# Kernel optimization log

Measured on AMD Instinct MI355X. Metric: run time of the kernel, lower is better.

## Reference

```python
import jax, jax.numpy as jnp
import numpy as np


def setup_inputs() -> dict:
    key = jax.random.key(0)
    k1, k2, k3 = jax.random.split(key, 3)
    B, T, C = 16, 8192, 128  # batch, tokens, max_columns
    column_logits = jax.random.normal(k1, (B, T, C), dtype=jnp.float32)
    column_assignments = jax.random.randint(k2, (B, T), 0, C)
    valid_mask = jax.random.randint(k3, (B, T), 0, 2).astype(bool)
    return {
        "column_logits": column_logits,
        "column_assignments": column_assignments,
        "valid_mask": valid_mask,
    }


def reference(column_logits, column_assignments, valid_mask):
    # column_logits: (B, T, C); column_assignments: (B, T) int; valid_mask: (B, T) bool
    B, T, C = column_logits.shape
    probs = jax.nn.softmax(column_logits, axis=-1).reshape(-1, C)  # (N, C)
    seg = column_assignments.reshape(-1)                           # (N,)
    w = valid_mask.reshape(-1).astype(probs.dtype)                 # (N,)

    # Single-pass segmented stats over column ids (num_segments = max_columns).
    n = jax.ops.segment_sum(w, seg, num_segments=C)                       # (C,)
    s = jax.ops.segment_sum(probs * w[:, None], seg, num_segments=C)      # (C, C)
    n_safe = jnp.maximum(n, 1.0)
    mean = s / n_safe[:, None]                                            # per-column mean prob

    # Sum of squared deviations (matches torch's ((p - mean)**2).mean()).
    diff = probs - mean[seg]
    ssd = jax.ops.segment_sum((diff * diff) * w[:, None], seg, num_segments=C)  # (C, C)
    col_var = ssd.sum(axis=-1) / (n_safe * C)                                    # (C,)

    has_multi = n > 1.0  # columns with at least 2 valid tokens
    count = has_multi.sum().astype(col_var.dtype)
    total = jnp.where(has_multi, col_var, 0.0).sum()
    return jnp.where(count > 0, total / jnp.maximum(count, 1.0), 0.0)
```

## Files before the change

kernel.cpp:

```cpp
#include <hip/hip_runtime.h>
#include <hip/hip_bf16.h>


#define NROWS 131072
#define CC    128
#define NB    256
#define RPB   512

typedef float f32x16 __attribute__((ext_vector_type(16)));
typedef short bf16x8 __attribute__((ext_vector_type(8)));

union U4V { uint4 u; bf16x8 v; };
union H2U { __hip_bfloat162 h; unsigned int u; };

__global__ __launch_bounds__(1024) void fused_kernel(
    const float* __restrict__ logits, const int* __restrict__ seg,
    const int* __restrict__ mask, float* __restrict__ slab_s,
    float* __restrict__ slab_n, float* __restrict__ slab_q,
    float* __restrict__ acc) {
  __shared__ ushort Plds[RPB * CC];
  __shared__ int sm[RPB];
  __shared__ unsigned int sg4[128];
  __shared__ float n_lds[CC], q_lds[CC];
  const int t = threadIdx.x, b = blockIdx.x;
  if (b == 0 && t < 4) ((unsigned int*)acc)[t] = 0u;
  if (t < CC) { n_lds[t] = 0.f; q_lds[t] = 0.f; }
  if (t < RPB) {
    const int r = b * RPB + t;
    sm[t] = seg[r] | (mask[r] << 16);
  }
  __syncthreads();
  if (t < 128) {
    unsigned int w = 0;
#pragma unroll
    for (int k = 0; k < 4; ++k) {
      const int smv = sm[t * 4 + k];
      const unsigned int sv = (smv >> 16) ? (unsigned int)(smv & 0xFFFF) : 255u;
      w |= sv << (8 * k);
    }
    sg4[t] = w;
  }

  const int wave = t >> 6, lane = t & 63;
  const int q = lane >> 5, j5 = lane & 31;
#pragma unroll
  for (int g = 0; g < 2; ++g) {
    const int ts = 2 * wave + g;
    const int rb = ts * 16 + q * 8;
    float x[8][4];
#pragma unroll
    for (int i = 0; i < 8; ++i) {
      const float* rp = logits + (size_t)(b * RPB + rb + i) * CC + j5;
#pragma unroll
      for (int nt = 0; nt < 4; ++nt) x[i][nt] = rp[nt * 32];
    }
    float inv[8], qr[8];
#pragma unroll
    for (int i = 0; i < 8; ++i) {
      float z = 0.f, z2 = 0.f;
#pragma unroll
      for (int nt = 0; nt < 4; ++nt) {
        const float e = __expf(x[i][nt]);
        x[i][nt] = e; z += e; z2 += e * e;
      }
#pragma unroll
      for (int off = 1; off < 32; off <<= 1) {
        z  += __shfl_xor(z, off, 64);
        z2 += __shfl_xor(z2, off, 64);
      }
      inv[i] = 1.0f / z;
      qr[i] = z2 * inv[i] * inv[i];
    }
#pragma unroll
    for (int nt = 0; nt < 4; ++nt) {
      unsigned int d[4];
#pragma unroll
      for (int k = 0; k < 4; ++k) {
        H2U h;
        h.h = __float22bfloat162_rn(make_float2(
            x[2 * k][nt] * inv[2 * k], x[2 * k + 1][nt] * inv[2 * k + 1]));
        d[k] = h.u;
      }
      *(uint4*)(Plds + ((size_t)(ts * 4 + nt) * 64 + lane) * 8) =
          make_uint4(d[0], d[1], d[2], d[3]);
    }
    if (j5 == 0) {
#pragma unroll
      for (int i = 0; i < 8; ++i) {
        const int smv = sm[rb + i];
        if (smv >> 16) {
          atomicAdd(&n_lds[smv & 0xFFFF], 1.0f);
          atomicAdd(&q_lds[smv & 0xFFFF], qr[i]);
        }
      }
    }
  }
  __syncthreads();

  if (t >= 256 && t < 384) slab_n[(t - 256) * NB + b] = n_lds[t - 256];
  else if (t >= 384 && t < 512) slab_q[(t - 384) * NB + b] = q_lds[t - 384];

  if (wave < 4) {
    const int mm = wave * 32 + (lane & 31);
    f32x16 acc0 = {}, acc1 = {}, acc2 = {}, acc3 = {};
    const ushort* pl = Plds + (size_t)lane * 8;
    for (int ks = 0; ks < 32; ++ks) {
      const unsigned int w0 = sg4[ks * 4 + q * 2];
      const unsigned int w1 = sg4[ks * 4 + q * 2 + 1];
      U4V a;
      {
        const unsigned int s0 = w0 & 255u, s1 = (w0 >> 8) & 255u;
        const unsigned int s2 = (w0 >> 16) & 255u, s3 = w0 >> 24;
        const unsigned int s4 = w1 & 255u, s5 = (w1 >> 8) & 255u;
        const unsigned int s6 = (w1 >> 16) & 255u, s7 = w1 >> 24;
        const unsigned int um = (unsigned int)mm;
        a.u = make_uint4(
            (s0 == um ? 0x3F80u : 0u) | (s1 == um ? 0x3F800000u : 0u),
            (s2 == um ? 0x3F80u : 0u) | (s3 == um ? 0x3F800000u : 0u),
            (s4 == um ? 0x3F80u : 0u) | (s5 == um ? 0x3F800000u : 0u),
            (s6 == um ? 0x3F80u : 0u) | (s7 == um ? 0x3F800000u : 0u));
      }
      U4V b0, b1, b2, b3;
      b0.u = *(const uint4*)(pl + (size_t)(ks * 4 + 0) * 512);
      b1.u = *(const uint4*)(pl + (size_t)(ks * 4 + 1) * 512);
      b2.u = *(const uint4*)(pl + (size_t)(ks * 4 + 2) * 512);
      b3.u = *(const uint4*)(pl + (size_t)(ks * 4 + 3) * 512);
      acc0 = __builtin_amdgcn_mfma_f32_32x32x16_bf16(a.v, b0.v, acc0, 0, 0, 0);
      acc1 = __builtin_amdgcn_mfma_f32_32x32x16_bf16(a.v, b1.v, acc1, 0, 0, 0);
      acc2 = __builtin_amdgcn_mfma_f32_32x32x16_bf16(a.v, b2.v, acc2, 0, 0, 0);
      acc3 = __builtin_amdgcn_mfma_f32_32x32x16_bf16(a.v, b3.v, acc3, 0, 0, 0);
    }
    float* outp = slab_s + (size_t)b * (CC * CC);
    const int jcol = lane & 31;
    const int rbase = (lane >> 5) * 4;
#pragma unroll
    for (int reg = 0; reg < 16; ++reg) {
      const int c = wave * 32 + (reg & 3) + 8 * (reg >> 2) + rbase;
      outp[c * CC + 0 * 32 + jcol] = acc0[reg];
      outp[c * CC + 1 * 32 + jcol] = acc1[reg];
      outp[c * CC + 2 * 32 + jcol] = acc2[reg];
      outp[c * CC + 3 * 32 + jcol] = acc3[reg];
    }
  }
}

__global__ __launch_bounds__(1024) void k3_colvar(
    const float* __restrict__ slab_s, const float* __restrict__ slab_n,
    const float* __restrict__ slab_q, float* __restrict__ acc,
    float* __restrict__ out) {
  const int c = blockIdx.x, t = threadIdx.x;
  const int v = t & 31, g0 = t >> 5;
  __shared__ float4 part[32][32];
  {
    const float4* base = (const float4*)slab_s +
                         (size_t)g0 * (CC * CC / 4) + c * (CC / 4) + v;
    float4 a = make_float4(0.f, 0.f, 0.f, 0.f);
#pragma unroll
    for (int i = 0; i < 8; ++i) {
      const float4 x = base[(size_t)(32 * i) * (CC * CC / 4)];
      a.x += x.x; a.y += x.y; a.z += x.z; a.w += x.w;
    }
    part[g0][v] = a;
  }
  float np = 0.f, qp = 0.f;
  if (t >= 64 && t < 128) {
    const int k = t - 64;
#pragma unroll
    for (int i = 0; i < 4; ++i) np += slab_n[c * NB + k + 64 * i];
  } else if (t >= 128 && t < 192) {
    const int k = t - 128;
#pragma unroll
    for (int i = 0; i < 4; ++i) qp += slab_q[c * NB + k + 64 * i];
  }
  __syncthreads();
  float tp = 0.f;
  if (t < 32) {
    float4 s = make_float4(0.f, 0.f, 0.f, 0.f);
#pragma unroll
    for (int g = 0; g < 32; ++g) {
      const float4 x = part[g][v];
      s.x += x.x; s.y += x.y; s.z += x.z; s.w += x.w;
    }
    tp = s.x * s.x + s.y * s.y + s.z * s.z + s.w * s.w;
  }
#pragma unroll
  for (int off = 1; off < 64; off <<= 1) {
    tp += __shfl_xor(tp, off, 64);
    np += __shfl_xor(np, off, 64);
    qp += __shfl_xor(qp, off, 64);
  }
  __shared__ float fin[3];
  if (t == 0) fin[0] = tp;
  else if (t == 64) fin[1] = np;
  else if (t == 128) fin[2] = qp;
  __syncthreads();
  if (t == 0) {
    const float tt = fin[0], nn = fin[1], qq = fin[2];
    float cv = 0.f, fl = 0.f;
    if (nn > 1.0f) {
      cv = (qq - tt / nn) / (nn * (float)CC);
      fl = 1.f;
    }
    atomicAdd(&acc[0], cv);
    atomicAdd(&acc[1], fl);
    __threadfence();
    const unsigned int old = atomicAdd((unsigned int*)&acc[2], 1u);
    if (old == (unsigned int)(CC - 1)) {
      const float total = atomicAdd(&acc[0], 0.f);
      const float count = atomicAdd(&acc[1], 0.f);
      out[0] = (count > 0.f) ? total / fmaxf(count, 1.f) : 0.f;
    }
  }
}

extern "C" void kernel_launch(void* const* d_in, const int* in_sizes, int n_in,
                              void* d_out, int out_size, void* d_ws,
                              size_t ws_size, hipStream_t stream) {
  const float* logits = (const float*)d_in[0];
  const int* seg = (const int*)d_in[1];
  const int* mask = (const int*)d_in[2];
  float* out = (float*)d_out;

  float* slab_s = (float*)d_ws;
  float* slab_n = slab_s + (size_t)NB * CC * CC;
  float* slab_q = slab_n + CC * NB;
  float* acc = slab_q + CC * NB;
  fused_kernel<<<NB, 1024, 0, stream>>>(logits, seg, mask, slab_s, slab_n,
                                        slab_q, acc);
  k3_colvar<<<CC, 1024, 0, stream>>>(slab_s, slab_n, slab_q, acc, out);
}
```

Measured before the change: 109.7 us.

## Pipeline softmax producers and MFMA consumers through a triple-buffered LDS ring

```diff
diff --git a/kernel.cpp b/kernel.cpp
--- a/kernel.cpp
+++ b/kernel.cpp
@@ -6,29 +6,101 @@
 #define CC    128
 #define NB    256
 #define RPB   512
+#define BUF_USHORTS (8 * 4 * 64 * 8)
 
 typedef float f32x16 __attribute__((ext_vector_type(16)));
 typedef short bf16x8 __attribute__((ext_vector_type(8)));
 
 union U4V { uint4 u; bf16x8 v; };
 union H2U { __hip_bfloat162 h; unsigned int u; };
+
+__device__ __forceinline__ float red32(float x) {
+  x += __int_as_float(__builtin_amdgcn_update_dpp(
+      0, __float_as_int(x), 0x121, 0xF, 0xF, true));
+  x += __int_as_float(__builtin_amdgcn_update_dpp(
+      0, __float_as_int(x), 0x122, 0xF, 0xF, true));
+  x += __int_as_float(__builtin_amdgcn_update_dpp(
+      0, __float_as_int(x), 0x124, 0xF, 0xF, true));
+  x += __int_as_float(__builtin_amdgcn_update_dpp(
+      0, __float_as_int(x), 0x128, 0xF, 0xF, true));
+  x += __int_as_float(
+      __builtin_amdgcn_ds_swizzle(__float_as_int(x), 0x401F));
+  return x;
+}
+
+__device__ __forceinline__ void load_x(const float* __restrict__ logits,
+                                       int b, int rb, int j5,
+                                       float (&x)[8][4]) {
+#pragma unroll
+  for (int i = 0; i < 8; ++i) {
+    const float* rp = logits + (size_t)(b * RPB + rb + i) * CC + j5;
+#pragma unroll
+    for (int nt = 0; nt < 4; ++nt) x[i][nt] = rp[nt * 32];
+  }
+}
+
+__device__ __forceinline__ void finish_ts(float (&x)[8][4], const int* sm,
+                                          float* n_lds, float* q_lds,
+                                          ushort* buf, int tsl, int rb,
+                                          int lane, int j5) {
+  float inv[8], qr[8];
+#pragma unroll
+  for (int i = 0; i < 8; ++i) {
+    float z = 0.f, z2 = 0.f;
+#pragma unroll
+    for (int nt = 0; nt < 4; ++nt) {
+      const float e = __expf(x[i][nt]);
+      x[i][nt] = e; z += e; z2 += e * e;
+    }
+    z = red32(z);
+    z2 = red32(z2);
+    inv[i] = 1.0f / z;
+    qr[i] = z2 * inv[i] * inv[i];
+  }
+#pragma unroll
+  for (int nt = 0; nt < 4; ++nt) {
+    unsigned int d[4];
+#pragma unroll
+    for (int k = 0; k < 4; ++k) {
+      H2U h;
+      h.h = __float22bfloat162_rn(make_float2(
+          x[2 * k][nt] * inv[2 * k], x[2 * k + 1][nt] * inv[2 * k + 1]));
+      d[k] = h.u;
+    }
+    *(uint4*)(buf + ((size_t)(tsl * 4 + nt) * 64 + lane) * 8) =
+        make_uint4(d[0], d[1], d[2], d[3]);
+  }
+  if (j5 == 0) {
+#pragma unroll
+    for (int i = 0; i < 8; ++i) {
+      const int smv = sm[rb + i];
+      if (smv >> 16) {
+        atomicAdd(&n_lds[smv & 0xFFFF], 1.0f);
+        atomicAdd(&q_lds[smv & 0xFFFF], qr[i]);
+      }
+    }
+  }
+}
 
 __global__ __launch_bounds__(1024) void fused_kernel(
     const float* __restrict__ logits, const int* __restrict__ seg,
     const int* __restrict__ mask, float* __restrict__ slab_s,
     float* __restrict__ slab_n, float* __restrict__ slab_q,
     float* __restrict__ acc) {
-  __shared__ ushort Plds[RPB * CC];
+  __shared__ ushort Pbuf[3][BUF_USHORTS];
   __shared__ int sm[RPB];
   __shared__ unsigned int sg4[128];
   __shared__ float n_lds[CC], q_lds[CC];
   const int t = threadIdx.x, b = blockIdx.x;
+  const int wave = t >> 6, lane = t & 63;
+  const int q = lane >> 5, j5 = lane & 31;
+
+  float x[8][4];
+  load_x(logits, b, wave * 16 + q * 8, j5, x);
+
   if (b == 0 && t < 4) ((unsigned int*)acc)[t] = 0u;
+  if (t < RPB) sm[t] = seg[b * RPB + t] | (mask[b * RPB + t] << 16);
   if (t < CC) { n_lds[t] = 0.f; q_lds[t] = 0.f; }
-  if (t < RPB) {
-    const int r = b * RPB + t;
-    sm[t] = seg[r] | (mask[r] << 16);
-  }
   __syncthreads();
   if (t < 128) {
     unsigned int w = 0;
@@ -40,106 +112,69 @@
     }
     sg4[t] = w;
   }
-
-  const int wave = t >> 6, lane = t & 63;
-  const int q = lane >> 5, j5 = lane & 31;
-#pragma unroll
-  for (int g = 0; g < 2; ++g) {
-    const int ts = 2 * wave + g;
-    const int rb = ts * 16 + q * 8;
-    float x[8][4];
-#pragma unroll
-    for (int i = 0; i < 8; ++i) {
-      const float* rp = logits + (size_t)(b * RPB + rb + i) * CC + j5;
-#pragma unroll
-      for (int nt = 0; nt < 4; ++nt) x[i][nt] = rp[nt * 32];
-    }
-    float inv[8], qr[8];
-#pragma unroll
-    for (int i = 0; i < 8; ++i) {
-      float z = 0.f, z2 = 0.f;
-#pragma unroll
-      for (int nt = 0; nt < 4; ++nt) {
-        const float e = __expf(x[i][nt]);
-        x[i][nt] = e; z += e; z2 += e * e;
+  finish_ts(x, sm, n_lds, q_lds, Pbuf[wave >> 3], wave & 7,
+            wave * 16 + q * 8, lane, j5);
+  __syncthreads();
+
+  const int ci = wave - 8;
+  const int m = ci & 3, nh = ci >> 2;
+  const int mm = m * 32 + (lane & 31);
+  f32x16 acc0 = {}, acc1 = {};
+
+#pragma unroll
+  for (int c = 0; c < 4; ++c) {
+    if (wave < 8) {
+      if (c < 2) {
+        const int ts = (c + 2) * 8 + wave;
+        float y[8][4];
+        load_x(logits, b, ts * 16 + q * 8, j5, y);
+        finish_ts(y, sm, n_lds, q_lds, Pbuf[(c + 2) % 3], wave,
+                  ts * 16 + q * 8, lane, j5);
+      } else if (c == 2) {
+        if (t < 128) slab_n[t * NB + b] = n_lds[t];
+        else if (t < 256) slab_q[(t - 128) * NB + b] = q_lds[t - 128];
       }
-#pragma unroll
-      for (int off = 1; off < 32; off <<= 1) {
-        z  += __shfl_xor(z, off, 64);
-        z2 += __shfl_xor(z2, off, 64);
+    } else {
+      const ushort* pl = Pbuf[c % 3] + (size_t)lane * 8;
+#pragma unroll
+      for (int tsl = 0; tsl < 8; ++tsl) {
+        const int ks = c * 8 + tsl;
+        const unsigned int w0 = sg4[ks * 4 + q * 2];
+        const unsigned int w1 = sg4[ks * 4 + q * 2 + 1];
+        U4V a;
+        {
+          const unsigned int s0 = w0 & 255u, s1 = (w0 >> 8) & 255u;
+          const unsigned int s2 = (w0 >> 16) & 255u, s3 = w0 >> 24;
+          const unsigned int s4 = w1 & 255u, s5 = (w1 >> 8) & 255u;
+          const unsigned int s6 = (w1 >> 16) & 255u, s7 = w1 >> 24;
+          const unsigned int um = (unsigned int)mm;
+          a.u = make_uint4(
+              (s0 == um ? 0x3F80u : 0u) | (s1 == um ? 0x3F800000u : 0u),
+              (s2 == um ? 0x3F80u : 0u) | (s3 == um ? 0x3F800000u : 0u),
+              (s4 == um ? 0x3F80u : 0u) | (s5 == um ? 0x3F800000u : 0u),
+              (s6 == um ? 0x3F80u : 0u) | (s7 == um ? 0x3F800000u : 0u));
+        }
+        U4V b0, b1;
+        b0.u = *(const uint4*)(pl + (size_t)(tsl * 4 + 2 * nh) * 512);
+        b1.u = *(const uint4*)(pl + (size_t)(tsl * 4 + 2 * nh + 1) * 512);
+        acc0 = __builtin_amdgcn_mfma_f32_32x32x16_bf16(a.v, b0.v, acc0,
+                                                       0, 0, 0);
+        acc1 = __builtin_amdgcn_mfma_f32_32x32x16_bf16(a.v, b1.v, acc1,
+                                                       0, 0, 0);
       }
-      inv[i] = 1.0f / z;
-      qr[i] = z2 * inv[i] * inv[i];
-    }
-#pragma unroll
-    for (int nt = 0; nt < 4; ++nt) {
-      unsigned int d[4];
-#pragma unroll
-      for (int k = 0; k < 4; ++k) {
-        H2U h;
-        h.h = __float22bfloat162_rn(make_float2(
-            x[2 * k][nt] * inv[2 * k], x[2 * k + 1][nt] * inv[2 * k + 1]));
-        d[k] = h.u;
-      }
-      *(uint4*)(Plds + ((size_t)(ts * 4 + nt) * 64 + lane) * 8) =
-          make_uint4(d[0], d[1], d[2], d[3]);
-    }
-    if (j5 == 0) {
-#pragma unroll
-      for (int i = 0; i < 8; ++i) {
-        const int smv = sm[rb + i];
-        if (smv >> 16) {
-          atomicAdd(&n_lds[smv & 0xFFFF], 1.0f);
-          atomicAdd(&q_lds[smv & 0xFFFF], qr[i]);
-        }
-      }
-    }
-  }
-  __syncthreads();
-
-  if (t >= 256 && t < 384) slab_n[(t - 256) * NB + b] = n_lds[t - 256];
-  else if (t >= 384 && t < 512) slab_q[(t - 384) * NB + b] = q_lds[t - 384];
-
-  if (wave < 4) {
-    const int mm = wave * 32 + (lane & 31);
-    f32x16 acc0 = {}, acc1 = {}, acc2 = {}, acc3 = {};
-    const ushort* pl = Plds + (size_t)lane * 8;
-    for (int ks = 0; ks < 32; ++ks) {
-      const unsigned int w0 = sg4[ks * 4 + q * 2];
-      const unsigned int w1 = sg4[ks * 4 + q * 2 + 1];
-      U4V a;
-      {
-        const unsigned int s0 = w0 & 255u, s1 = (w0 >> 8) & 255u;
-        const unsigned int s2 = (w0 >> 16) & 255u, s3 = w0 >> 24;
-        const unsigned int s4 = w1 & 255u, s5 = (w1 >> 8) & 255u;
-        const unsigned int s6 = (w1 >> 16) & 255u, s7 = w1 >> 24;
-        const unsigned int um = (unsigned int)mm;
-        a.u = make_uint4(
-            (s0 == um ? 0x3F80u : 0u) | (s1 == um ? 0x3F800000u : 0u),
-            (s2 == um ? 0x3F80u : 0u) | (s3 == um ? 0x3F800000u : 0u),
-            (s4 == um ? 0x3F80u : 0u) | (s5 == um ? 0x3F800000u : 0u),
-            (s6 == um ? 0x3F80u : 0u) | (s7 == um ? 0x3F800000u : 0u));
-      }
-      U4V b0, b1, b2, b3;
-      b0.u = *(const uint4*)(pl + (size_t)(ks * 4 + 0) * 512);
-      b1.u = *(const uint4*)(pl + (size_t)(ks * 4 + 1) * 512);
-      b2.u = *(const uint4*)(pl + (size_t)(ks * 4 + 2) * 512);
-      b3.u = *(const uint4*)(pl + (size_t)(ks * 4 + 3) * 512);
-      acc0 = __builtin_amdgcn_mfma_f32_32x32x16_bf16(a.v, b0.v, acc0, 0, 0, 0);
-      acc1 = __builtin_amdgcn_mfma_f32_32x32x16_bf16(a.v, b1.v, acc1, 0, 0, 0);
-      acc2 = __builtin_amdgcn_mfma_f32_32x32x16_bf16(a.v, b2.v, acc2, 0, 0, 0);
-      acc3 = __builtin_amdgcn_mfma_f32_32x32x16_bf16(a.v, b3.v, acc3, 0, 0, 0);
-    }
+    }
+    if (c < 3) __syncthreads();
+  }
+
+  if (wave >= 8) {
     float* outp = slab_s + (size_t)b * (CC * CC);
     const int jcol = lane & 31;
     const int rbase = (lane >> 5) * 4;
 #pragma unroll
     for (int reg = 0; reg < 16; ++reg) {
-      const int c = wave * 32 + (reg & 3) + 8 * (reg >> 2) + rbase;
-      outp[c * CC + 0 * 32 + jcol] = acc0[reg];
-      outp[c * CC + 1 * 32 + jcol] = acc1[reg];
-      outp[c * CC + 2 * 32 + jcol] = acc2[reg];
-      outp[c * CC + 3 * 32 + jcol] = acc3[reg];
+      const int cr = m * 32 + (reg & 3) + 8 * (reg >> 2) + rbase;
+      outp[cr * CC + (2 * nh) * 32 + jcol] = acc0[reg];
+      outp[cr * CC + (2 * nh + 1) * 32 + jcol] = acc1[reg];
     }
   }
 }
@@ -157,8 +192,8 @@
     float4 a = make_float4(0.f, 0.f, 0.f, 0.f);
 #pragma unroll
     for (int i = 0; i < 8; ++i) {
-      const float4 x = base[(size_t)(32 * i) * (CC * CC / 4)];
-      a.x += x.x; a.y += x.y; a.z += x.z; a.w += x.w;
+      const float4 xx = base[(size_t)(32 * i) * (CC * CC / 4)];
+      a.x += xx.x; a.y += xx.y; a.z += xx.z; a.w += xx.w;
     }
     part[g0][v] = a;
   }
@@ -178,8 +213,8 @@
     float4 s = make_float4(0.f, 0.f, 0.f, 0.f);
 #pragma unroll
     for (int g = 0; g < 32; ++g) {
-      const float4 x = part[g][v];
-      s.x += x.x; s.y += x.y; s.z += x.z; s.w += x.w;
+      const float4 xx = part[g][v];
+      s.x += xx.x; s.y += xx.y; s.z += xx.z; s.w += xx.w;
     }
     tp = s.x * s.x + s.y * s.y + s.z * s.z + s.w * s.w;
   }
```

New measurement: 111.4 us. Within noise of the previous version (+1.6%).

## Vectorize logits loads, use DPP reductions, and swizzle LDS probability layout

Applied to the files above, without the earlier changes.

```diff
diff --git a/kernel.cpp b/kernel.cpp
--- a/kernel.cpp
+++ b/kernel.cpp
@@ -12,6 +12,20 @@
 
 union U4V { uint4 u; bf16x8 v; };
 union H2U { __hip_bfloat162 h; unsigned int u; };
+
+__device__ __forceinline__ float red32(float x) {
+  x += __int_as_float(__builtin_amdgcn_update_dpp(
+      0, __float_as_int(x), 0x121, 0xF, 0xF, true));
+  x += __int_as_float(__builtin_amdgcn_update_dpp(
+      0, __float_as_int(x), 0x122, 0xF, 0xF, true));
+  x += __int_as_float(__builtin_amdgcn_update_dpp(
+      0, __float_as_int(x), 0x124, 0xF, 0xF, true));
+  x += __int_as_float(__builtin_amdgcn_update_dpp(
+      0, __float_as_int(x), 0x128, 0xF, 0xF, true));
+  x += __int_as_float(
+      __builtin_amdgcn_ds_swizzle(__float_as_int(x), 0x401F));
+  return x;
+}
 
 __global__ __launch_bounds__(1024) void fused_kernel(
     const float* __restrict__ logits, const int* __restrict__ seg,
@@ -43,46 +57,47 @@
 
   const int wave = t >> 6, lane = t & 63;
   const int q = lane >> 5, j5 = lane & 31;
+  const int swz = ((j5 >> 1) & 3) << 4;
+  char* const pb0 = (char*)Plds + q * 512 + (j5 & 7) * 64;
+
 #pragma unroll
   for (int g = 0; g < 2; ++g) {
     const int ts = 2 * wave + g;
     const int rb = ts * 16 + q * 8;
+    const float4* rp4 =
+        (const float4*)(logits + (size_t)(b * RPB + rb) * CC) + j5;
     float x[8][4];
 #pragma unroll
     for (int i = 0; i < 8; ++i) {
-      const float* rp = logits + (size_t)(b * RPB + rb + i) * CC + j5;
-#pragma unroll
-      for (int nt = 0; nt < 4; ++nt) x[i][nt] = rp[nt * 32];
+      const float4 v = rp4[i * 32];
+      x[i][0] = v.x; x[i][1] = v.y; x[i][2] = v.z; x[i][3] = v.w;
     }
     float inv[8], qr[8];
 #pragma unroll
     for (int i = 0; i < 8; ++i) {
       float z = 0.f, z2 = 0.f;
 #pragma unroll
-      for (int nt = 0; nt < 4; ++nt) {
-        const float e = __expf(x[i][nt]);
-        x[i][nt] = e; z += e; z2 += e * e;
-      }
-#pragma unroll
-      for (int off = 1; off < 32; off <<= 1) {
-        z  += __shfl_xor(z, off, 64);
-        z2 += __shfl_xor(z2, off, 64);
-      }
+      for (int m = 0; m < 4; ++m) {
+        const float e = __expf(x[i][m]);
+        x[i][m] = e; z += e; z2 += e * e;
+      }
+      z = red32(z);
+      z2 = red32(z2);
       inv[i] = 1.0f / z;
       qr[i] = z2 * inv[i] * inv[i];
     }
-#pragma unroll
-    for (int nt = 0; nt < 4; ++nt) {
+    char* const pbt = pb0 + (size_t)(ts * 4 + (j5 >> 3)) * 1024;
+#pragma unroll
+    for (int m = 0; m < 4; ++m) {
       unsigned int d[4];
 #pragma unroll
       for (int k = 0; k < 4; ++k) {
         H2U h;
         h.h = __float22bfloat162_rn(make_float2(
-            x[2 * k][nt] * inv[2 * k], x[2 * k + 1][nt] * inv[2 * k + 1]));
+            x[2 * k][m] * inv[2 * k], x[2 * k + 1][m] * inv[2 * k + 1]));
         d[k] = h.u;
       }
-      *(uint4*)(Plds + ((size_t)(ts * 4 + nt) * 64 + lane) * 8) =
-          make_uint4(d[0], d[1], d[2], d[3]);
+      *(uint4*)(pbt + ((m * 16) ^ swz)) = make_uint4(d[0], d[1], d[2], d[3]);
     }
     if (j5 == 0) {
 #pragma unroll
@@ -103,7 +118,9 @@
   if (wave < 4) {
     const int mm = wave * 32 + (lane & 31);
     f32x16 acc0 = {}, acc1 = {}, acc2 = {}, acc3 = {};
-    const ushort* pl = Plds + (size_t)lane * 8;
+    const int nrd = lane & 31;
+    const char* pl = (char*)Plds +
+        ((q * 512 + nrd * 16) ^ (((nrd >> 3) & 3) << 4));
     for (int ks = 0; ks < 32; ++ks) {
       const unsigned int w0 = sg4[ks * 4 + q * 2];
       const unsigned int w1 = sg4[ks * 4 + q * 2 + 1];
@@ -121,10 +138,10 @@
             (s6 == um ? 0x3F80u : 0u) | (s7 == um ? 0x3F800000u : 0u));
       }
       U4V b0, b1, b2, b3;
-      b0.u = *(const uint4*)(pl + (size_t)(ks * 4 + 0) * 512);
-      b1.u = *(const uint4*)(pl + (size_t)(ks * 4 + 1) * 512);
-      b2.u = *(const uint4*)(pl + (size_t)(ks * 4 + 2) * 512);
-      b3.u = *(const uint4*)(pl + (size_t)(ks * 4 + 3) * 512);
+      b0.u = *(const uint4*)(pl + (size_t)(ks * 4 + 0) * 1024);
+      b1.u = *(const uint4*)(pl + (size_t)(ks * 4 + 1) * 1024);
+      b2.u = *(const uint4*)(pl + (size_t)(ks * 4 + 2) * 1024);
+      b3.u = *(const uint4*)(pl + (size_t)(ks * 4 + 3) * 1024);
       acc0 = __builtin_amdgcn_mfma_f32_32x32x16_bf16(a.v, b0.v, acc0, 0, 0, 0);
       acc1 = __builtin_amdgcn_mfma_f32_32x32x16_bf16(a.v, b1.v, acc1, 0, 0, 0);
       acc2 = __builtin_amdgcn_mfma_f32_32x32x16_bf16(a.v, b2.v, acc2, 0, 0, 0);
@@ -157,8 +174,8 @@
     float4 a = make_float4(0.f, 0.f, 0.f, 0.f);
 #pragma unroll
     for (int i = 0; i < 8; ++i) {
-      const float4 x = base[(size_t)(32 * i) * (CC * CC / 4)];
-      a.x += x.x; a.y += x.y; a.z += x.z; a.w += x.w;
+      const float4 xx = base[(size_t)(32 * i) * (CC * CC / 4)];
+      a.x += xx.x; a.y += xx.y; a.z += xx.z; a.w += xx.w;
     }
     part[g0][v] = a;
   }
@@ -178,8 +195,8 @@
     float4 s = make_float4(0.f, 0.f, 0.f, 0.f);
 #pragma unroll
     for (int g = 0; g < 32; ++g) {
-      const float4 x = part[g][v];
-      s.x += x.x; s.y += x.y; s.z += x.z; s.w += x.w;
+      const float4 xx = part[g][v];
+      s.x += xx.x; s.y += xx.y; s.z += xx.z; s.w += xx.w;
     }
     tp = s.x * s.x + s.y * s.y + s.z * s.z + s.w * s.w;
   }
```

Result: no change. 110.8 us (+1.0%).
